# Kernel optimization log

Hardware: AMD Instinct MI355X
Metric: run time of the kernel (lower is better)

Reference implementation:

```python
import jax, jax.numpy as jnp
import numpy as np

K = 32          # neighbors_for_lrf
EPS = 1e-12     # safe-sqrt epsilon (self-distance is exactly 0)


def shot_lrf(neighborhoods, radii):
    """SHOT local reference frames.
    neighborhoods: (N, K, 3) neighbor offsets (neighbor - center)
    radii:         (N,) support radius (distance to farthest of the K neighbors)
    returns        (N, 3, 3) rows = [x, y, z] axes
    """
    k = neighborhoods.shape[1]
    dists = jnp.sqrt(jnp.maximum(jnp.sum(neighborhoods ** 2, axis=-1), EPS))  # (N,K)
    w = radii[:, None] - dists                                                # (N,K) SHOT weights
    cov = jnp.einsum("nk,nki,nkj->nij", w, neighborhoods, neighborhoods)
    cov = cov / jnp.sum(w, axis=-1)[:, None, None]                            # (N,3,3)

    _, evecs = jnp.linalg.eigh(cov)            # ascending eigenvalues
    x = evecs[:, :, 2]                          # largest-eigenvalue eigenvector
    z = evecs[:, :, 0]                          # smallest-eigenvalue eigenvector

    # Sign disambiguation: orient axis toward the majority of neighbors.
    px = jnp.einsum("nki,ni->nk", neighborhoods, x)
    n_pos_x = jnp.sum(px >= 0, axis=-1)
    x = jnp.where((n_pos_x >= k - n_pos_x)[:, None], x, -x)

    pz = jnp.einsum("nki,ni->nk", neighborhoods, z)
    n_pos_z = jnp.sum(pz >= 0, axis=-1)
    z = jnp.where((n_pos_z >= k - n_pos_z)[:, None], z, -z)

    y = jnp.cross(z, x)
    return jnp.stack([x, y, z], axis=1)         # (N,3,3)


def knn_shot_lrf(k, verts):
    """verts: (N,3) -> (N,3,3) LRFs via KNN + weighted-covariance eigendecomposition."""
    d2 = jnp.sum((verts[:, None, :] - verts[None, :, :]) ** 2, axis=-1)  # (N,N)
    dist = jnp.sqrt(jnp.maximum(d2, EPS))
    neg_top, idx = jax.lax.top_k(-dist, k)      # k nearest (includes self)
    radii = -neg_top[:, -1]                     # distance to farthest kept neighbor
    nbh = verts[idx] - verts[:, None, :]        # (N,K,3) gathered, centered neighborhoods
    return shot_lrf(nbh, radii)


def setup_inputs() -> dict:
    key = jax.random.key(0)
    vertices = jax.random.normal(key, (2, 8192, 3), dtype=jnp.float32)
    return {"vertices": vertices}


def reference(vertices):
    B, N = vertices.shape[0], vertices.shape[1]
    lrfs = jax.vmap(lambda v: knn_shot_lrf(K, v))(vertices)  # (B,N,3,3)
    return lrfs.reshape(B, N, 9)
```

## Files before the change

### kernel.cpp

```cpp
#include <hip/hip_runtime.h>
#include <stdint.h>

#define NPTS 8192
#define KNN  32
#define WAVES 8
#define BTHR (WAVES*64)
#define CAP  512
#define K2BLK 64

#define EPSF    5.9604645e-08f
#define EPS2F   3.5527137e-15f
#define SAFMINF 1.17549435e-38f
#define SAFMAXF 8.5070592e+37f
#define RTMINF  1.0842022e-19f
#define RTMAXF  9.2233720e+18f

__device__ __forceinline__ float fsignf(float a, float b) {
  return __builtin_copysignf(fabsf(a), b);
}

__device__ __forceinline__ float slapy2f(float x, float y) {
  float xa = fabsf(x), ya = fabsf(y);
  float w = fmaxf(xa, ya), z = fminf(xa, ya);
  if (z == 0.0f) return w;
  float t = __fdiv_rn(z, w);
  return __fmul_rn(w, __fsqrt_rn(__fadd_rn(1.0f, __fmul_rn(t, t))));
}

__device__ __forceinline__ void slartgf(float f, float g, float& c, float& s, float& r) {
  if (g == 0.0f)      { c = 1.0f; s = 0.0f; r = f; }
  else if (f == 0.0f) { c = 0.0f; s = __builtin_copysignf(1.0f, g); r = fabsf(g); }
  else {
    float f1 = fabsf(f), g1 = fabsf(g);
    if (f1 > RTMINF && f1 < RTMAXF && g1 > RTMINF && g1 < RTMAXF) {
      float d = __fsqrt_rn(__fadd_rn(__fmul_rn(f, f), __fmul_rn(g, g)));
      c = __fdiv_rn(f1, d);
      r = __builtin_copysignf(d, f);
      s = __fdiv_rn(g, r);
    } else {
      float u  = fminf(SAFMAXF, fmaxf(SAFMINF, fmaxf(f1, g1)));
      float fs = __fdiv_rn(f, u), gs = __fdiv_rn(g, u);
      float d  = __fsqrt_rn(__fadd_rn(__fmul_rn(fs, fs), __fmul_rn(gs, gs)));
      c = __fdiv_rn(fabsf(fs), d);
      r = __builtin_copysignf(d, f);
      s = __fdiv_rn(gs, r);
      r = __fmul_rn(r, u);
    }
  }
}

__device__ void slaev2f(float a, float b, float c,
                        float& rt1, float& rt2, float& cs1, float& sn1) {
  float sm = __fadd_rn(a, c), df = __fsub_rn(a, c);
  float adf = fabsf(df), tb = __fadd_rn(b, b), ab = fabsf(tb);
  float acmx, acmn;
  if (fabsf(a) > fabsf(c)) { acmx = a; acmn = c; } else { acmx = c; acmn = a; }
  float rt;
  if (adf > ab) {
    float t = __fdiv_rn(ab, adf);
    rt = __fmul_rn(adf, __fsqrt_rn(__fadd_rn(1.0f, __fmul_rn(t, t))));
  } else if (adf < ab) {
    float t = __fdiv_rn(adf, ab);
    rt = __fmul_rn(ab, __fsqrt_rn(__fadd_rn(1.0f, __fmul_rn(t, t))));
  } else {
    rt = __fmul_rn(ab, __fsqrt_rn(2.0f));
  }
  int sgn1;
  if (sm < 0.0f) {
    rt1 = __fmul_rn(0.5f, __fsub_rn(sm, rt)); sgn1 = -1;
    rt2 = __fsub_rn(__fmul_rn(__fdiv_rn(acmx, rt1), acmn), __fmul_rn(__fdiv_rn(b, rt1), b));
  } else if (sm > 0.0f) {
    rt1 = __fmul_rn(0.5f, __fadd_rn(sm, rt)); sgn1 = 1;
    rt2 = __fsub_rn(__fmul_rn(__fdiv_rn(acmx, rt1), acmn), __fmul_rn(__fdiv_rn(b, rt1), b));
  } else {
    rt1 = __fmul_rn(0.5f, rt); rt2 = -rt1; sgn1 = 1;
  }
  float cs; int sgn2;
  if (df >= 0.0f) { cs = __fadd_rn(df, rt); sgn2 = 1; }
  else            { cs = __fsub_rn(df, rt); sgn2 = -1; }
  float acs = fabsf(cs);
  if (acs > ab) {
    float ct = __fdiv_rn(-tb, cs);
    sn1 = __fdiv_rn(1.0f, __fsqrt_rn(__fadd_rn(1.0f, __fmul_rn(ct, ct))));
    cs1 = __fmul_rn(ct, sn1);
  } else {
    if (ab == 0.0f) { cs1 = 1.0f; sn1 = 0.0f; }
    else {
      float tn = __fdiv_rn(-cs, tb);
      cs1 = __fdiv_rn(1.0f, __fsqrt_rn(__fadd_rn(1.0f, __fmul_rn(tn, tn))));
      sn1 = __fmul_rn(tn, cs1);
    }
  }
  if (sgn1 == sgn2) { float tn = cs1; cs1 = -sn1; sn1 = tn; }
}

#define ZZ(i,j) base[((i)*3+(j))*K2BLK]
#define DD(i)   base[(9+(i))*K2BLK]
#define EE(i)   base[(12+(i))*K2BLK]
#define CW(i)   base[(14+(i))*K2BLK]
#define SW(i)   base[(16+(i))*K2BLK]

__device__ void steqr3f(float* base) {
  const int nmaxit = 90;
  int jtot = 0;
  int l1 = 0;
  for (int outer = 0; outer < 6; ++outer) {
    if (l1 > 2) break;
    if (l1 > 0) EE(l1 - 1) = 0.0f;
    int m = 2;
    for (int mm = l1; mm <= 1; ++mm) {
      float tst = fabsf(EE(mm));
      if (tst == 0.0f) { m = mm; break; }
      float thr = __fmul_rn(__fmul_rn(__fsqrt_rn(fabsf(DD(mm))), __fsqrt_rn(fabsf(DD(mm + 1)))), EPSF);
      if (tst <= thr) { EE(mm) = 0.0f; m = mm; break; }
    }
    int l = l1;
    int lend = m;
    l1 = m + 1;
    if (lend == l) continue;
    if (fabsf(DD(lend)) < fabsf(DD(l))) { int t = l; l = lend; lend = t; }
    if (lend > l) {
      for (int it = 0; it < 120; ++it) {
        int m2 = lend;
        if (l != lend) {
          for (int mm = l; mm <= lend - 1; ++mm) {
            float tst = __fmul_rn(EE(mm), EE(mm));
            float thr = __fadd_rn(__fmul_rn(__fmul_rn(EPS2F, fabsf(DD(mm))), fabsf(DD(mm + 1))), SAFMINF);
            if (tst <= thr) { m2 = mm; break; }
          }
        }
        if (m2 < lend) EE(m2) = 0.0f;
        float p = DD(l);
        if (m2 == l) {
          DD(l) = p; l += 1;
          if (l <= lend) continue;
          break;
        }
        if (m2 == l + 1) {
          float rt1, rt2, cc, ss;
          slaev2f(DD(l), EE(l), DD(l + 1), rt1, rt2, cc, ss);
          for (int i = 0; i < 3; ++i) {
            float tz = ZZ(i, l + 1);
            ZZ(i, l + 1) = __fsub_rn(__fmul_rn(cc, tz), __fmul_rn(ss, ZZ(i, l)));
            ZZ(i, l)     = __fadd_rn(__fmul_rn(ss, tz), __fmul_rn(cc, ZZ(i, l)));
          }
          DD(l) = rt1; DD(l + 1) = rt2; EE(l) = 0.0f;
          l += 2;
          if (l <= lend) continue;
          break;
        }
        if (jtot == nmaxit) break;
        jtot++;
        float g = __fdiv_rn(__fsub_rn(DD(l + 1), p), __fmul_rn(2.0f, EE(l)));
        float r = slapy2f(g, 1.0f);
        g = __fadd_rn(__fsub_rn(DD(m2), p), __fdiv_rn(EE(l), __fadd_rn(g, fsignf(r, g))));
        float s = 1.0f, c = 1.0f;
        p = 0.0f;
        for (int i = m2 - 1; i >= l; --i) {
          float f = __fmul_rn(s, EE(i));
          float b = __fmul_rn(c, EE(i));
          slartgf(g, f, c, s, r);
          if (i != m2 - 1) EE(i + 1) = r;
          g = __fsub_rn(DD(i + 1), p);
          r = __fadd_rn(__fmul_rn(__fsub_rn(DD(i), g), s), __fmul_rn(__fmul_rn(2.0f, c), b));
          p = __fmul_rn(s, r);
          DD(i + 1) = __fadd_rn(g, p);
          g = __fsub_rn(__fmul_rn(c, r), b);
          CW(i - l) = c; SW(i - l) = -s;
        }
        int mmc = m2 - l + 1;
        for (int j = mmc - 2; j >= 0; --j) {
          float cj = CW(j), sj = SW(j);
          for (int i = 0; i < 3; ++i) {
            float tz = ZZ(i, l + j + 1);
            ZZ(i, l + j + 1) = __fsub_rn(__fmul_rn(cj, tz), __fmul_rn(sj, ZZ(i, l + j)));
            ZZ(i, l + j)     = __fadd_rn(__fmul_rn(sj, tz), __fmul_rn(cj, ZZ(i, l + j)));
          }
        }
        DD(l) = __fsub_rn(DD(l), p);
        EE(l) = g;
      }
    } else {
      for (int it = 0; it < 120; ++it) {
        int m2 = lend;
        if (l != lend) {
          for (int mm = l; mm >= lend + 1; --mm) {
            float tst = __fmul_rn(EE(mm - 1), EE(mm - 1));
            float thr = __fadd_rn(__fmul_rn(__fmul_rn(EPS2F, fabsf(DD(mm))), fabsf(DD(mm - 1))), SAFMINF);
            if (tst <= thr) { m2 = mm; break; }
          }
        }
        if (m2 > lend) EE(m2 - 1) = 0.0f;
        float p = DD(l);
        if (m2 == l) {
          DD(l) = p; l -= 1;
          if (l >= lend) continue;
          break;
        }
        if (m2 == l - 1) {
          float rt1, rt2, cc, ss;
          slaev2f(DD(l - 1), EE(l - 1), DD(l), rt1, rt2, cc, ss);
          for (int i = 0; i < 3; ++i) {
            float tz = ZZ(i, l);
            ZZ(i, l)     = __fsub_rn(__fmul_rn(cc, tz), __fmul_rn(ss, ZZ(i, l - 1)));
            ZZ(i, l - 1) = __fadd_rn(__fmul_rn(ss, tz), __fmul_rn(cc, ZZ(i, l - 1)));
          }
          DD(l - 1) = rt1; DD(l) = rt2; EE(l - 1) = 0.0f;
          l -= 2;
          if (l >= lend) continue;
          break;
        }
        if (jtot == nmaxit) break;
        jtot++;
        float g = __fdiv_rn(__fsub_rn(DD(l - 1), p), __fmul_rn(2.0f, EE(l - 1)));
        float r = slapy2f(g, 1.0f);
        g = __fadd_rn(__fsub_rn(DD(m2), p), __fdiv_rn(EE(l - 1), __fadd_rn(g, fsignf(r, g))));
        float s = 1.0f, c = 1.0f;
        p = 0.0f;
        for (int i = m2; i <= l - 1; ++i) {
          float f = __fmul_rn(s, EE(i));
          float b = __fmul_rn(c, EE(i));
          slartgf(g, f, c, s, r);
          if (i != m2) EE(i - 1) = r;
          g = __fsub_rn(DD(i), p);
          r = __fadd_rn(__fmul_rn(__fsub_rn(DD(i + 1), g), s), __fmul_rn(__fmul_rn(2.0f, c), b));
          p = __fmul_rn(s, r);
          DD(i) = __fadd_rn(g, p);
          g = __fsub_rn(__fmul_rn(c, r), b);
          CW(i - m2) = c; SW(i - m2) = s;
        }
        int mmc = l - m2 + 1;
        for (int j = 0; j <= mmc - 2; ++j) {
          float cj = CW(j), sj = SW(j);
          for (int i = 0; i < 3; ++i) {
            float tz = ZZ(i, m2 + j + 1);
            ZZ(i, m2 + j + 1) = __fsub_rn(__fmul_rn(cj, tz), __fmul_rn(sj, ZZ(i, m2 + j)));
            ZZ(i, m2 + j)     = __fadd_rn(__fmul_rn(sj, tz), __fmul_rn(cj, ZZ(i, m2 + j)));
          }
        }
        DD(l) = __fsub_rn(DD(l), p);
        EE(l - 1) = g;
      }
    }
    if (jtot >= nmaxit) break;
  }
  for (int ii = 1; ii < 3; ++ii) {
    int i = ii - 1, k = i;
    float p = DD(i);
    for (int j = ii; j < 3; ++j) {
      if (DD(j) < p) { k = j; p = DD(j); }
    }
    if (k != i) {
      DD(k) = DD(i); DD(i) = p;
      for (int r = 0; r < 3; ++r) { float t = ZZ(r, i); ZZ(r, i) = ZZ(r, k); ZZ(r, k) = t; }
    }
  }
}

__device__ __forceinline__ uint32_t d2_ubound(float T) {
  float t2 = __fmul_rn(T, T);
  uint32_t u = __float_as_uint(fmaxf(t2, 0.0f));
  for (int i = 0; i < 64 && u > 0; ++i) {
    if (__fsqrt_rn(fmaxf(__uint_as_float(u), 1e-12f)) <= T) break;
    --u;
  }
  for (int i = 0; i < 64; ++i) {
    if (!(__fsqrt_rn(fmaxf(__uint_as_float(u + 1), 1e-12f)) <= T)) break;
    ++u;
  }
  return u;
}


__global__ __launch_bounds__(BTHR)
void knn_select_kernel(const float* __restrict__ verts, uint32_t* __restrict__ nbr) {
  __shared__ uint64_t SURV[WAVES * CAP];

  const int tid  = threadIdx.x;
  const int w    = tid >> 6;
  const int lane = tid & 63;
  const int query = blockIdx.x * WAVES + w;
  const int b  = query >> 13;
  const int qi = query & (NPTS - 1);
  const float* vb = verts + (size_t)b * NPTS * 3;

  const float qx = vb[3 * qi + 0], qy = vb[3 * qi + 1], qz = vb[3 * qi + 2];

  float sd[4];
#pragma unroll
  for (int s = 0; s < 4; ++s) {
    int j = s * 64 + lane;
    float dxx = __fsub_rn(vb[3 * j + 0], qx);
    float dyy = __fsub_rn(vb[3 * j + 1], qy);
    float dzz = __fsub_rn(vb[3 * j + 2], qz);
    float d2 = __fadd_rn(__fadd_rn(__fmul_rn(dxx, dxx), __fmul_rn(dyy, dyy)), __fmul_rn(dzz, dzz));
    sd[s] = __fsqrt_rn(fmaxf(d2, 1e-12f));
  }
  {
    float lo, hi;
    lo = fminf(sd[0], sd[1]); hi = fmaxf(sd[0], sd[1]); sd[0] = lo; sd[1] = hi;
    lo = fminf(sd[2], sd[3]); hi = fmaxf(sd[2], sd[3]); sd[2] = lo; sd[3] = hi;
    lo = fminf(sd[0], sd[2]); hi = fmaxf(sd[0], sd[2]); sd[0] = lo; sd[2] = hi;
    lo = fminf(sd[1], sd[3]); hi = fmaxf(sd[1], sd[3]); sd[1] = lo; sd[3] = hi;
    lo = fminf(sd[1], sd[2]); hi = fmaxf(sd[1], sd[2]); sd[1] = lo; sd[2] = hi;
  }
  const float INF = __builtin_inff();
  float T = 0.0f;
  for (int r = 0; r < 6; ++r) {
    float g = sd[0];
    for (int o = 32; o; o >>= 1) g = fminf(g, __shfl_xor(g, o));
    bool win = (sd[0] == g) && (g < INF);
    sd[0] = win ? sd[1] : sd[0];
    sd[1] = win ? sd[2] : sd[1];
    sd[2] = win ? sd[3] : sd[2];
    sd[3] = win ? INF   : sd[3];
    if (g < INF) T = g;
  }

  const uint64_t lmask_lt = (lane == 0) ? 0ull : (~0ull >> (64 - lane));
  uint32_t U = d2_ubound(T);
  int cnt = 0;
  for (int attempt = 0; attempt < 8; ++attempt) {
    cnt = 0;
#pragma unroll 8
    for (int s = 0; s < NPTS / 64; ++s) {
      int j = s * 64 + lane;
      float dxx = __fsub_rn(vb[3 * j + 0], qx);
      float dyy = __fsub_rn(vb[3 * j + 1], qy);
      float dzz = __fsub_rn(vb[3 * j + 2], qz);
      float d2 = __fadd_rn(__fadd_rn(__fmul_rn(dxx, dxx), __fmul_rn(dyy, dyy)), __fmul_rn(dzz, dzz));
      uint32_t D2 = __float_as_uint(d2);
      bool p = (D2 <= U);
      uint64_t m = __ballot(p);
      if (p) {
        int off = cnt + (int)__popcll(m & lmask_lt);
        if (off < CAP) SURV[w * CAP + off] = ((uint64_t)D2 << 32) | (uint32_t)j;
      }
      cnt += (int)__popcll(m);
    }
    if (cnt > CAP)      { T = __fmul_rn(T, 0.7f); U = d2_ubound(T); continue; }
    else if (cnt < KNN) { T = __fmul_rn(T, 1.8f); U = d2_ubound(T); continue; }
    break;
  }

  uint32_t myidx = 0xFFFFFFFFu;
  const bool fast_ok = (cnt >= KNN && cnt <= CAP);
  if (fast_ok) {
    const int n = cnt;
    uint64_t kr[8];
#pragma unroll
    for (int t = 0; t < 8; ++t) {
      int idx = lane + (t << 6);
      if (idx < n) {
        uint64_t v = SURV[w * CAP + idx];
        float dist = __fsqrt_rn(fmaxf(__uint_as_float((uint32_t)(v >> 32)), 1e-12f));
        kr[t] = ((uint64_t)__float_as_uint(dist) << 32) | (uint32_t)v;
      } else {
        kr[t] = ~0ull;
      }
    }
    uint64_t last = 0;
    for (int r = 0; r < KNN; ++r) {
      uint64_t lmin = ~0ull;
#pragma unroll
      for (int t = 0; t < 8; ++t) {
        uint64_t v = kr[t];
        if (v > last && v < lmin) lmin = v;
      }
      uint64_t g = lmin;
      for (int o = 32; o; o >>= 1) {
        uint64_t t2 = __shfl_xor((unsigned long long)g, o);
        if (t2 < g) g = t2;
      }
      if (lane == r) myidx = (uint32_t)g;
      last = g;
    }
  } else {
    uint64_t last = 0;
    for (int r = 0; r < KNN; ++r) {
      uint64_t lmin = ~0ull;
      for (int s = 0; s < NPTS / 64; ++s) {
        int j = s * 64 + lane;
        float dxx = __fsub_rn(vb[3 * j + 0], qx);
        float dyy = __fsub_rn(vb[3 * j + 1], qy);
        float dzz = __fsub_rn(vb[3 * j + 2], qz);
        float d2 = __fadd_rn(__fadd_rn(__fmul_rn(dxx, dxx), __fmul_rn(dyy, dyy)), __fmul_rn(dzz, dzz));
        uint64_t key = ((uint64_t)__float_as_uint(__fsqrt_rn(fmaxf(d2, 1e-12f))) << 32) | (uint32_t)j;
        if (key > last && key < lmin) lmin = key;
      }
      uint64_t g = lmin;
      for (int o = 32; o; o >>= 1) {
        uint64_t t2 = __shfl_xor((unsigned long long)g, o);
        if (t2 < g) g = t2;
      }
      if (lane == r) myidx = (uint32_t)g;
      last = g;
    }
  }

  if (lane < KNN) nbr[(size_t)query * KNN + lane] = myidx;
}


__global__ __launch_bounds__(K2BLK)
void shot_lrf_kernel(const float* __restrict__ verts,
                     const uint32_t* __restrict__ nbr,
                     float* __restrict__ out) {
  __shared__ float EW[18 * K2BLK];

  const int tid = threadIdx.x;
  const int query = blockIdx.x * K2BLK + tid;
  const int b  = query >> 13;
  const int qi = query & (NPTS - 1);
  const float* vb = verts + (size_t)b * NPTS * 3;

  const float qx = vb[3 * qi + 0], qy = vb[3 * qi + 1], qz = vb[3 * qi + 2];

  uint32_t idxs[KNN];
#pragma unroll
  for (int k = 0; k < KNN; ++k)
    idxs[k] = nbr[(size_t)query * KNN + k] & (NPTS - 1);

  float radii;
  {
    int i31 = (int)idxs[KNN - 1];
    float dxx = __fsub_rn(vb[3 * i31 + 0], qx);
    float dyy = __fsub_rn(vb[3 * i31 + 1], qy);
    float dzz = __fsub_rn(vb[3 * i31 + 2], qz);
    float d2 = __fadd_rn(__fadd_rn(__fmul_rn(dxx, dxx), __fmul_rn(dyy, dyy)), __fmul_rn(dzz, dzz));
    radii = __fsqrt_rn(fmaxf(d2, 1e-12f));
  }

  float rr[8];
#pragma unroll
  for (int i = 0; i < 8; ++i) rr[i] = 0.0f;
  float l00[4], l10[4], l20[4], l11[4], l21[4], l22[4];
#pragma unroll
  for (int L = 0; L < 4; ++L) { l00[L]=0.0f; l10[L]=0.0f; l20[L]=0.0f; l11[L]=0.0f; l21[L]=0.0f; l22[L]=0.0f; }
#pragma unroll
  for (int c = 0; c < 8; ++c) {
#pragma unroll
    for (int L = 0; L < 4; ++L) {
      int k2 = 4 * c + L;
      int idx = (int)idxs[k2];
      float dxx = __fsub_rn(vb[3 * idx + 0], qx);
      float dyy = __fsub_rn(vb[3 * idx + 1], qy);
      float dzz = __fsub_rn(vb[3 * idx + 2], qz);
      float d2 = __fadd_rn(__fadd_rn(__fmul_rn(dxx, dxx), __fmul_rn(dyy, dyy)), __fmul_rn(dzz, dzz));
      float dist = __fsqrt_rn(fmaxf(d2, 1e-12f));
      float wgt = __fsub_rn(radii, dist);
      rr[k2 & 7] = __fadd_rn(rr[k2 & 7], wgt);
      float wx = __fmul_rn(wgt, dxx), wy = __fmul_rn(wgt, dyy), wz = __fmul_rn(wgt, dzz);
      l00[L] = __fadd_rn(l00[L], __fmul_rn(wx, dxx));
      l10[L] = __fadd_rn(l10[L], __fmul_rn(wy, dxx));
      l20[L] = __fadd_rn(l20[L], __fmul_rn(wz, dxx));
      l11[L] = __fadd_rn(l11[L], __fmul_rn(wy, dyy));
      l21[L] = __fadd_rn(l21[L], __fmul_rn(wz, dyy));
      l22[L] = __fadd_rn(l22[L], __fmul_rn(wz, dzz));
    }
  }
  float c00 = __fadd_rn(__fadd_rn(l00[0], l00[1]), __fadd_rn(l00[2], l00[3]));
  float c10 = __fadd_rn(__fadd_rn(l10[0], l10[1]), __fadd_rn(l10[2], l10[3]));
  float c20 = __fadd_rn(__fadd_rn(l20[0], l20[1]), __fadd_rn(l20[2], l20[3]));
  float c11 = __fadd_rn(__fadd_rn(l11[0], l11[1]), __fadd_rn(l11[2], l11[3]));
  float c21 = __fadd_rn(__fadd_rn(l21[0], l21[1]), __fadd_rn(l21[2], l21[3]));
  float c22 = __fadd_rn(__fadd_rn(l22[0], l22[1]), __fadd_rn(l22[2], l22[3]));
  float sumw = __fadd_rn(
      __fadd_rn(__fadd_rn(rr[0], rr[1]), __fadd_rn(rr[2], rr[3])),
      __fadd_rn(__fadd_rn(rr[4], rr[5]), __fadd_rn(rr[6], rr[7])));

  float a11 = __fdiv_rn(c00, sumw);
  float a21 = __fdiv_rn(c10, sumw);
  float a31 = __fdiv_rn(c20, sumw);
  float a22 = __fdiv_rn(c11, sumw);
  float a32 = __fdiv_rn(c21, sumw);
  float a33 = __fdiv_rn(c22, sumw);

  float* base = &EW[tid];
  float taui, v2;
  {
    float alpha = a21;
    float xnorm = fabsf(a31);
    float beta;
    if (xnorm == 0.0f) {
      taui = 0.0f; v2 = 0.0f; beta = alpha;
      DD(0) = a11; DD(1) = a22; DD(2) = a33;
      EE(0) = beta; EE(1) = a32;
    } else {
      beta = -fsignf(slapy2f(alpha, xnorm), alpha);
      taui = __fdiv_rn(__fsub_rn(beta, alpha), beta);
      float inv = __fdiv_rn(1.0f, __fsub_rn(alpha, beta));
      v2 = __fmul_rn(a31, inv);
      float y1 = __fmul_rn(taui, a22);
      float y2 = __fmul_rn(taui, a32);
      float temp2 = __fmul_rn(a32, v2);
      y1 = __fadd_rn(y1, __fmul_rn(taui, temp2));
      y2 = __fadd_rn(y2, __fmul_rn(__fmul_rn(taui, v2), a33));
      float dot = __fadd_rn(y1, __fmul_rn(y2, v2));
      float aw = __fmul_rn(__fmul_rn(-0.5f, taui), dot);
      float w1 = __fadd_rn(y1, aw);
      float w2 = __fadd_rn(y2, __fmul_rn(aw, v2));
      float a22p = __fadd_rn(__fadd_rn(a22, __fmul_rn(1.0f, -w1)), __fmul_rn(w1, -1.0f));
      float a32p = __fadd_rn(__fadd_rn(a32, __fmul_rn(v2, -w1)), __fmul_rn(w2, -1.0f));
      float a33p = __fadd_rn(__fadd_rn(a33, __fmul_rn(v2, -w2)), __fmul_rn(w2, -v2));
      DD(0) = a11; DD(1) = a22p; DD(2) = a33p;
      EE(0) = beta; EE(1) = a32p;
    }
  }

  for (int i = 0; i < 3; ++i)
    for (int j = 0; j < 3; ++j)
      ZZ(i, j) = (i == j) ? 1.0f : 0.0f;

  steqr3f(base);

  if (taui != 0.0f) {
    for (int j = 0; j < 3; ++j) {
      float wj = __fadd_rn(ZZ(1, j), __fmul_rn(ZZ(2, j), v2));
      float t = __fmul_rn(-taui, wj);
      ZZ(1, j) = __fadd_rn(ZZ(1, j), t);
      ZZ(2, j) = __fadd_rn(ZZ(2, j), __fmul_rn(v2, t));
    }
  }

  float X0 = ZZ(0, 2), X1 = ZZ(1, 2), X2 = ZZ(2, 2);
  float Z0 = ZZ(0, 0), Z1 = ZZ(1, 0), Z2 = ZZ(2, 0);

  int npx = 0, npz = 0;
#pragma unroll
  for (int k2 = 0; k2 < KNN; ++k2) {
    int idx = (int)idxs[k2];
    float dxx = __fsub_rn(vb[3 * idx + 0], qx);
    float dyy = __fsub_rn(vb[3 * idx + 1], qy);
    float dzz = __fsub_rn(vb[3 * idx + 2], qz);
    float px = __fadd_rn(__fadd_rn(__fmul_rn(dxx, X0), __fmul_rn(dyy, X1)), __fmul_rn(dzz, X2));
    float pz = __fadd_rn(__fadd_rn(__fmul_rn(dxx, Z0), __fmul_rn(dyy, Z1)), __fmul_rn(dzz, Z2));
    if (px >= 0.0f) npx++;
    if (pz >= 0.0f) npz++;
  }
  if (2 * npx < KNN) { X0 = -X0; X1 = -X1; X2 = -X2; }
  if (2 * npz < KNN) { Z0 = -Z0; Z1 = -Z1; Z2 = -Z2; }

  float Y0 = __fsub_rn(__fmul_rn(Z1, X2), __fmul_rn(Z2, X1));
  float Y1 = __fsub_rn(__fmul_rn(Z2, X0), __fmul_rn(Z0, X2));
  float Y2 = __fsub_rn(__fmul_rn(Z0, X1), __fmul_rn(Z1, X0));

  float* o = out + (size_t)query * 9;
  o[0] = X0; o[1] = X1; o[2] = X2;
  o[3] = Y0; o[4] = Y1; o[5] = Y2;
  o[6] = Z0; o[7] = Z1; o[8] = Z2;
}

#undef ZZ
#undef DD
#undef EE
#undef CW
#undef SW

extern "C" void kernel_launch(void* const* d_in, const int* in_sizes, int n_in,
                              void* d_out, int out_size, void* d_ws, size_t ws_size,
                              hipStream_t stream) {
  (void)n_in; (void)out_size; (void)ws_size;
  const float* verts = (const float*)d_in[0];
  float* out = (float*)d_out;
  uint32_t* nbr = (uint32_t*)d_ws;
  int total = in_sizes[0] / 3;
  knn_select_kernel<<<total / WAVES, BTHR, 0, stream>>>(verts, nbr);
  shot_lrf_kernel<<<total / K2BLK, K2BLK, 0, stream>>>(verts, nbr, out);
}
```

Baseline: 175.5 us.

## Bucket points into a uniform spatial grid to prune KNN candidate scans

Builds a per-batch 32^3 uniform grid with histogram, three-stage prefix scan and scatter kernels, storing points in SoA sorted by cell. The KNN threshold pass now visits only cells overlapping the query's bounding box instead of scanning all 8192 points, and falls back to the brute-force path when too many cell rows are touched. Neighbor indices are also narrowed to 16-bit. This adds several small kernel launches and atomics per call in exchange for far fewer distance evaluations.

```diff
diff --git a/kernel.cpp b/kernel.cpp
--- a/kernel.cpp
+++ b/kernel.cpp
@@ -7,6 +7,12 @@
 #define BTHR (WAVES*64)
 #define CAP  512
 #define K2BLK 64
+
+#define G     32
+#define NCELL 32768
+#define TOTC  65536
+#define GLO   (-6.0f)
+#define GINV  (2.6666667f)
 
 #define EPSF    5.9604645e-08f
 #define EPS2F   3.5527137e-15f
@@ -271,9 +277,83 @@
   return u;
 }
 
+__device__ __forceinline__ int cellf(float x) {
+  int c = (int)floorf(__fmul_rn(__fsub_rn(x, GLO), GINV));
+  return c < 0 ? 0 : (c > (G - 1) ? (G - 1) : c);
+}
+
+
+__global__ __launch_bounds__(256)
+void hist_kernel(const float* __restrict__ verts, uint32_t* __restrict__ cnt) {
+  int i = blockIdx.x * 256 + threadIdx.x;
+  const float* p = verts + (size_t)i * 3;
+  uint32_t c = (uint32_t)(i >> 13) * (uint32_t)NCELL +
+               (((uint32_t)cellf(p[2]) * G + (uint32_t)cellf(p[1])) * G + (uint32_t)cellf(p[0]));
+  atomicAdd(&cnt[c], 1u);
+}
+
+__global__ __launch_bounds__(1024)
+void scanA_kernel(const uint32_t* __restrict__ cnt, uint32_t* __restrict__ start,
+                  uint32_t* __restrict__ bsum) {
+  __shared__ uint32_t sh[1024];
+  int t = threadIdx.x;
+  int g = blockIdx.x * 1024 + t;
+  uint32_t v = cnt[g];
+  sh[t] = v;
+  __syncthreads();
+  for (int off = 1; off < 1024; off <<= 1) {
+    uint32_t u = (t >= off) ? sh[t - off] : 0u;
+    __syncthreads();
+    sh[t] += u;
+    __syncthreads();
+  }
+  start[g] = sh[t] - v;
+  if (t == 1023) bsum[blockIdx.x] = sh[1023];
+}
+
+__global__ __launch_bounds__(64)
+void scanB_kernel(uint32_t* __restrict__ bsum, uint32_t* __restrict__ start) {
+  int lane = threadIdx.x;
+  uint32_t v = bsum[lane];
+  uint32_t inc = v;
+  for (int off = 1; off < 64; off <<= 1) {
+    uint32_t t = __shfl_up(inc, off);
+    if (lane >= off) inc += t;
+  }
+  bsum[lane] = inc - v;
+  if (lane == 63) start[TOTC] = inc;
+}
+
+__global__ __launch_bounds__(1024)
+void scanC_kernel(uint32_t* __restrict__ start, const uint32_t* __restrict__ bsum,
+                  uint32_t* __restrict__ cursor) {
+  int g = blockIdx.x * 1024 + threadIdx.x;
+  start[g] += bsum[blockIdx.x];
+  cursor[g] = 0u;
+}
+
+__global__ __launch_bounds__(256)
+void scatter_kernel(const float* __restrict__ verts, const uint32_t* __restrict__ start,
+                    uint32_t* __restrict__ cursor,
+                    float* __restrict__ sx, float* __restrict__ sy, float* __restrict__ sz,
+                    uint16_t* __restrict__ sidx) {
+  int i = blockIdx.x * 256 + threadIdx.x;
+  const float* p = verts + (size_t)i * 3;
+  float px = p[0], py = p[1], pz = p[2];
+  uint32_t c = (uint32_t)(i >> 13) * (uint32_t)NCELL +
+               (((uint32_t)cellf(pz) * G + (uint32_t)cellf(py)) * G + (uint32_t)cellf(px));
+  uint32_t slot = start[c] + atomicAdd(&cursor[c], 1u);
+  sx[slot] = px; sy[slot] = py; sz[slot] = pz;
+  sidx[slot] = (uint16_t)(i & (NPTS - 1));
+}
+
 
 __global__ __launch_bounds__(BTHR)
-void knn_select_kernel(const float* __restrict__ verts, uint32_t* __restrict__ nbr) {
+void knn_select_kernel(const float* __restrict__ verts,
+                       const uint32_t* __restrict__ cellstart,
+                       const float* __restrict__ sx, const float* __restrict__ sy,
+                       const float* __restrict__ sz, const uint16_t* __restrict__ sidx,
+                       uint16_t* __restrict__ nbr) {
   __shared__ uint64_t SURV[WAVES * CAP];
 
   const int tid  = threadIdx.x;
@@ -319,24 +399,40 @@
 
   const uint64_t lmask_lt = (lane == 0) ? 0ull : (~0ull >> (64 - lane));
   uint32_t U = d2_ubound(T);
+  const uint32_t cbase = (uint32_t)b * (uint32_t)NCELL;
   int cnt = 0;
+  bool fast = true;
   for (int attempt = 0; attempt < 8; ++attempt) {
+    float Tq = __fmul_rn(T, 1.00001f);
+    int cx0 = cellf(__fsub_rn(qx, Tq)), cx1 = cellf(__fadd_rn(qx, Tq));
+    int cy0 = cellf(__fsub_rn(qy, Tq)), cy1 = cellf(__fadd_rn(qy, Tq));
+    int cz0 = cellf(__fsub_rn(qz, Tq)), cz1 = cellf(__fadd_rn(qz, Tq));
+    int npairs = (cy1 - cy0 + 1) * (cz1 - cz0 + 1);
+    if (npairs > 192) { fast = false; break; }
     cnt = 0;
-#pragma unroll 8
-    for (int s = 0; s < NPTS / 64; ++s) {
-      int j = s * 64 + lane;
-      float dxx = __fsub_rn(vb[3 * j + 0], qx);
-      float dyy = __fsub_rn(vb[3 * j + 1], qy);
-      float dzz = __fsub_rn(vb[3 * j + 2], qz);
-      float d2 = __fadd_rn(__fadd_rn(__fmul_rn(dxx, dxx), __fmul_rn(dyy, dyy)), __fmul_rn(dzz, dzz));
-      uint32_t D2 = __float_as_uint(d2);
-      bool p = (D2 <= U);
-      uint64_t m = __ballot(p);
-      if (p) {
-        int off = cnt + (int)__popcll(m & lmask_lt);
-        if (off < CAP) SURV[w * CAP + off] = ((uint64_t)D2 << 32) | (uint32_t)j;
-      }
-      cnt += (int)__popcll(m);
+    for (int cz = cz0; cz <= cz1; ++cz) {
+      for (int cy = cy0; cy <= cy1; ++cy) {
+        uint32_t row = cbase + ((uint32_t)cz * G + (uint32_t)cy) * G;
+        uint32_t sbeg = cellstart[row + (uint32_t)cx0];
+        uint32_t send = cellstart[row + (uint32_t)cx1 + 1];
+        for (uint32_t i0 = sbeg; i0 < send; i0 += 64) {
+          uint32_t i = i0 + (uint32_t)lane;
+          bool inb = (i < send);
+          uint32_t ii = inb ? i : sbeg;
+          float dxx = __fsub_rn(sx[ii], qx);
+          float dyy = __fsub_rn(sy[ii], qy);
+          float dzz = __fsub_rn(sz[ii], qz);
+          float d2 = __fadd_rn(__fadd_rn(__fmul_rn(dxx, dxx), __fmul_rn(dyy, dyy)), __fmul_rn(dzz, dzz));
+          uint32_t D2 = __float_as_uint(d2);
+          bool p = inb && (D2 <= U);
+          uint64_t m = __ballot(p);
+          if (p) {
+            int off = cnt + (int)__popcll(m & lmask_lt);
+            if (off < CAP) SURV[w * CAP + off] = ((uint64_t)D2 << 32) | (uint32_t)sidx[ii];
+          }
+          cnt += (int)__popcll(m);
+        }
+      }
     }
     if (cnt > CAP)      { T = __fmul_rn(T, 0.7f); U = d2_ubound(T); continue; }
     else if (cnt < KNN) { T = __fmul_rn(T, 1.8f); U = d2_ubound(T); continue; }
@@ -344,7 +440,7 @@
   }
 
   uint32_t myidx = 0xFFFFFFFFu;
-  const bool fast_ok = (cnt >= KNN && cnt <= CAP);
+  const bool fast_ok = fast && (cnt >= KNN && cnt <= CAP);
   if (fast_ok) {
     const int n = cnt;
     uint64_t kr[8];
@@ -398,13 +494,13 @@
     }
   }
 
-  if (lane < KNN) nbr[(size_t)query * KNN + lane] = myidx;
+  if (lane < KNN) nbr[(size_t)query * KNN + lane] = (uint16_t)myidx;
 }
 
 
 __global__ __launch_bounds__(K2BLK)
 void shot_lrf_kernel(const float* __restrict__ verts,
-                     const uint32_t* __restrict__ nbr,
+                     const uint16_t* __restrict__ nbr,
                      float* __restrict__ out) {
   __shared__ float EW[18 * K2BLK];
 
@@ -419,7 +515,7 @@
   uint32_t idxs[KNN];
 #pragma unroll
   for (int k = 0; k < KNN; ++k)
-    idxs[k] = nbr[(size_t)query * KNN + k] & (NPTS - 1);
+    idxs[k] = (uint32_t)nbr[(size_t)query * KNN + k] & (NPTS - 1);
 
   float radii;
   {
@@ -563,8 +659,24 @@
   (void)n_in; (void)out_size; (void)ws_size;
   const float* verts = (const float*)d_in[0];
   float* out = (float*)d_out;
-  uint32_t* nbr = (uint32_t*)d_ws;
   int total = in_sizes[0] / 3;
-  knn_select_kernel<<<total / WAVES, BTHR, 0, stream>>>(verts, nbr);
+
+  char* ws = (char*)d_ws;
+  uint16_t* nbr    = (uint16_t*)(ws);
+  uint32_t* cstart = (uint32_t*)(ws + 1048576);
+  uint32_t* ccnt   = (uint32_t*)(ws + 1048576 + 262400);
+  uint32_t* bsum   = (uint32_t*)(ws + 1048576 + 262400 + 262144);
+  float*    sx     = (float*)   (ws + 1048576 + 262400 + 262144 + 256);
+  float*    sy     = sx + 16384;
+  float*    sz     = sy + 16384;
+  uint16_t* sidx   = (uint16_t*)(sz + 16384);
+
+  hipMemsetAsync(ccnt, 0, (size_t)TOTC * 4, stream);
+  hist_kernel   <<<total / 256, 256, 0, stream>>>(verts, ccnt);
+  scanA_kernel  <<<TOTC / 1024, 1024, 0, stream>>>(ccnt, cstart, bsum);
+  scanB_kernel  <<<1, 64, 0, stream>>>(bsum, cstart);
+  scanC_kernel  <<<TOTC / 1024, 1024, 0, stream>>>(cstart, bsum, ccnt);
+  scatter_kernel<<<total / 256, 256, 0, stream>>>(verts, cstart, ccnt, sx, sy, sz, sidx);
+  knn_select_kernel<<<total / WAVES, BTHR, 0, stream>>>(verts, cstart, sx, sy, sz, sidx, nbr);
   shot_lrf_kernel<<<total / K2BLK, K2BLK, 0, stream>>>(verts, nbr, out);
 }
```

New measurement: 434.4 us. +147.5%, slower.
